# Kernel optimization log

Hardware: AMD Instinct MI355X
Metric: run time of the kernel (lower is better)

Reference implementation:

```python
import jax, jax.numpy as jnp
import numpy as np

N, E, B = 50000, 600000, 64
C_IN, H, C_OUT, L = 128, 128, 64, 3
BN_EPS = 1e-5


def setup_inputs() -> dict:
    key = jax.random.key(0)
    ks = iter(jax.random.split(key, 40))

    def w(shape, fan_in):
        return jax.random.normal(next(ks), shape, jnp.float32) / np.sqrt(fan_in).astype(np.float32)

    return {
        "x": jax.random.normal(next(ks), (N, C_IN), jnp.float32),
        "edge_index": jax.random.randint(next(ks), (2, E), 0, N),
        "batch": jnp.sort(jax.random.randint(next(ks), (N,), 0, B)),
        # GINConv MLPs: Linear(in,h) -> BN -> ReLU -> Linear(h,h)   (stacked over L; C_IN == H)
        "convW1": w((L, C_IN, H), C_IN), "convb1": jnp.zeros((L, H), jnp.float32),
        "bn_g": jnp.ones((L, H), jnp.float32), "bn_b": jnp.zeros((L, H), jnp.float32),
        "convW2": w((L, H, H), H), "convb2": jnp.zeros((L, H), jnp.float32),
        # reconstruction head: Linear(h,h)-ReLU-Linear(h,h)-ReLU-Linear(h,4)-ReLU
        "recW1": w((H, H), H), "recb1": jnp.zeros((H,), jnp.float32),
        "recW2": w((H, H), H), "recb2": jnp.zeros((H,), jnp.float32),
        "recW3": w((H, 4), H), "recb3": jnp.zeros((4,), jnp.float32),
        # final MLP([h,h,out], norm=None): Linear(h,h)-ReLU-(dropout, eval=identity)-Linear(h,out)
        "mlpW1": w((H, H), H), "mlpb1": jnp.zeros((H,), jnp.float32),
        "mlpW2": w((H, C_OUT), H), "mlpb2": jnp.zeros((C_OUT,), jnp.float32),
    }


def reference(x, edge_index, batch, convW1, convb1, bn_g, bn_b, convW2, convb2,
              recW1, recb1, recW2, recb2, recW3, recb3, mlpW1, mlpb1, mlpW2, mlpb2):
    src, dst = edge_index[0], edge_index[1]
    for l in range(L):
        # GIN aggregation: out_i = nn((1+eps)*x_i + sum_{j->i} x_j), eps = 0
        agg = jax.ops.segment_sum(x[src], dst, num_segments=N)  # [N, d]
        h = (x + agg) @ convW1[l] + convb1[l]                   # [N, H]
        mu = h.mean(axis=0)
        var = jnp.var(h, axis=0)                                # biased, torch BN train mode
        h = bn_g[l] * (h - mu) * jax.lax.rsqrt(var + BN_EPS) + bn_b[l]
        h = jax.nn.relu(h) @ convW2[l] + convb2[l]
        x = jax.nn.relu(h)                                      # outer .relu() in forward
    # reconstruction branch on node features
    x_rec = jax.nn.relu(x @ recW1 + recb1)
    x_rec = jax.nn.relu(x_rec @ recW2 + recb2)
    x_rec = jax.nn.relu(x_rec @ recW3 + recb3)                  # [N, 4]
    # global_add_pool keyed by graph id
    pooled = jax.ops.segment_sum(x, batch, num_segments=B)      # [B, H]
    out = jax.nn.relu(pooled @ mlpW1 + mlpb1) @ mlpW2 + mlpb2   # [B, C_OUT]
    return (out, x_rec)
```

## Files before the change

kernel.cpp:

```cpp
#include <hip/hip_runtime.h>

#define NN 50000
#define EE 600000
#define BB 64
#define CH 128
#define LL 3
#define NGB 391
#define NSB 196
#define NPB 392

typedef unsigned short u16;
typedef unsigned int u32;
typedef short s16x8 __attribute__((ext_vector_type(8)));
typedef float f32x4 __attribute__((ext_vector_type(4)));

__device__ __forceinline__ u16 f2b(float f) {
    u32 x = __float_as_uint(f);
    return (u16)((x + 0x7FFFu + ((x >> 16) & 1u)) >> 16);
}
__device__ __forceinline__ float b2f(u16 u) {
    return __uint_as_float(((u32)u) << 16);
}

__global__ __launch_bounds__(256) void k_zero2(int* __restrict__ deg,
                                               float* __restrict__ pooled,
                                               float* __restrict__ gstats,
                                               int* __restrict__ bar) {
    int i = blockIdx.x * 256 + threadIdx.x;
    if (i < NN) deg[i] = 0;
    int j = i - NN;
    if (j >= 0 && j < BB * CH) pooled[j] = 0.f;
    int k = j - BB * CH;
    if (k >= 0 && k < 3 * 256) gstats[k] = 0.f;
    int l = k - 3 * 256;
    if (l >= 0 && l < 4) bar[l] = 0;
}

__global__ __launch_bounds__(256) void k_count(const int* __restrict__ ei,
                                               int* __restrict__ deg) {
    int e = blockIdx.x * 256 + threadIdx.x;
    if (e < EE) atomicAdd(&deg[ei[EE + e]], 1);
}

__global__ __launch_bounds__(256) void k_scanA(const int* __restrict__ deg,
                                               int* __restrict__ bsum) {
    __shared__ int sm[256];
    int i = blockIdx.x * 256 + threadIdx.x;
    sm[threadIdx.x] = (i < NN) ? deg[i] : 0;
    __syncthreads();
    for (int off = 128; off > 0; off >>= 1) {
        if (threadIdx.x < off) sm[threadIdx.x] += sm[threadIdx.x + off];
        __syncthreads();
    }
    if (threadIdx.x == 0) bsum[blockIdx.x] = sm[0];
}

__global__ __launch_bounds__(256) void k_scanB(const int* __restrict__ deg,
                                               const int* __restrict__ bsum,
                                               int* __restrict__ rowptr,
                                               int* __restrict__ cur) {
    __shared__ int sb[256], sd[256];
    int t = threadIdx.x;
    sb[t] = (t < NSB) ? bsum[t] : 0;
    __syncthreads();
    for (int off = 1; off < 256; off <<= 1) {
        int v = (t >= off) ? sb[t - off] : 0;
        __syncthreads();
        sb[t] += v;
        __syncthreads();
    }
    int blockOff = (blockIdx.x == 0) ? 0 : sb[blockIdx.x - 1];
    int i = blockIdx.x * 256 + t;
    int d = (i < NN) ? deg[i] : 0;
    sd[t] = d;
    __syncthreads();
    for (int off = 1; off < 256; off <<= 1) {
        int v = (t >= off) ? sd[t - off] : 0;
        __syncthreads();
        sd[t] += v;
        __syncthreads();
    }
    int excl = blockOff + sd[t] - d;
    if (i < NN) { rowptr[i] = excl; cur[i] = excl; }
    if (i == NN - 1) rowptr[NN] = excl + d;
}

__global__ __launch_bounds__(256) void k_fill(const int* __restrict__ ei,
                                              int* __restrict__ cur,
                                              int* __restrict__ perm) {
    int e = blockIdx.x * 256 + threadIdx.x;
    if (e < EE) {
        int dst = ei[EE + e];
        int idx = atomicAdd(&cur[dst], 1);
        perm[idx] = ei[e];
    }
}

__global__ __launch_bounds__(256) void k_cvt(const float* __restrict__ x,
                                             u16* __restrict__ y) {
    long base = (long)(blockIdx.x * 256 + threadIdx.x) * 8;
    if (base < (long)NN * CH) {
        float4 f0 = *(const float4*)(x + base);
        float4 f1 = *(const float4*)(x + base + 4);
        union { u16 pk[8]; uint4 v; } uu;
        uu.pk[0] = f2b(f0.x); uu.pk[1] = f2b(f0.y);
        uu.pk[2] = f2b(f0.z); uu.pk[3] = f2b(f0.w);
        uu.pk[4] = f2b(f1.x); uu.pk[5] = f2b(f1.y);
        uu.pk[6] = f2b(f1.z); uu.pk[7] = f2b(f1.w);
        *(uint4*)(y + base) = uu.v;
    }
}

__global__ __launch_bounds__(256) void k_gather(const u16* __restrict__ x,
                                                const int* __restrict__ rowptr,
                                                const int* __restrict__ perm,
                                                u16* __restrict__ y) {
    int dst = blockIdx.x * 16 + (threadIdx.x >> 4);
    if (dst >= NN) return;
    int lane = threadIdx.x & 15;
    int co = lane * 8;
    int beg = rowptr[dst], end = rowptr[dst + 1];
    union { u16 pk[8]; uint4 v; } uu;
    uu.v = *(const uint4*)(x + (long)dst * CH + co);
    float a[8], b[8];
#pragma unroll
    for (int j = 0; j < 8; ++j) { a[j] = b2f(uu.pk[j]); b[j] = 0.f; }
    int e = beg;
    for (; e + 1 < end; e += 2) {
        int s0 = perm[e], s1 = perm[e + 1];
        union { u16 pk[8]; uint4 v; } v0, v1;
        v0.v = *(const uint4*)(x + (long)s0 * CH + co);
        v1.v = *(const uint4*)(x + (long)s1 * CH + co);
#pragma unroll
        for (int j = 0; j < 8; ++j) { a[j] += b2f(v0.pk[j]); b[j] += b2f(v1.pk[j]); }
    }
    if (e < end) {
        int s0 = perm[e];
        union { u16 pk[8]; uint4 v; } v0;
        v0.v = *(const uint4*)(x + (long)s0 * CH + co);
#pragma unroll
        for (int j = 0; j < 8; ++j) a[j] += b2f(v0.pk[j]);
    }
    union { u16 pk[8]; uint4 v; } ov;
#pragma unroll
    for (int j = 0; j < 8; ++j) ov.pk[j] = f2b(a[j] + b[j]);
    *(uint4*)(y + (long)dst * CH + co) = ov.v;
}

__global__ __launch_bounds__(256) void k_transpose_all(
    const float* __restrict__ cW1, const float* __restrict__ cW2,
    const float* __restrict__ rW1, const float* __restrict__ rW2,
    const float* __restrict__ rW3, u16* __restrict__ Wt) {
    int idx = blockIdx.x * 256 + threadIdx.x;
    if (idx < 8 * 16384) {
        int slot = idx >> 14;
        int wi = idx & 16383;
        int k = wi >> 7, n = wi & 127;
        const float* src = slot < 3 ? cW1 + slot * 16384
                         : slot < 6 ? cW2 + (slot - 3) * 16384
                         : slot == 6 ? rW1 : rW2;
        Wt[slot * 16384 + n * 128 + k] = f2b(src[wi]);
    } else if (idx < 9 * 16384) {
        int j = idx - 8 * 16384;
        int n = j >> 7, k = j & 127;
        Wt[8 * 16384 + j] = (n < 4) ? f2b(rW3[k * 4 + n]) : (u16)0;
    }
}

__device__ __forceinline__ void stageB8(const u16* __restrict__ Wt, u16* sB,
                                        int s, int rr) {
#pragma unroll
    for (int it = 0; it < 8; ++it) {
        int n = it * 16 + rr;
        uint4 u = *(const uint4*)(Wt + n * CH + 8 * s);
        *(uint4*)(&sB[n * CH + ((s ^ (n & 15)) * 8)]) = u;
    }
}

__device__ __forceinline__ void mfma8(const u16* sA, const u16* sB,
                                      f32x4 acc[2][8], int wv, int quad, int l16) {
    f32x4 z = {0.f, 0.f, 0.f, 0.f};
#pragma unroll
    for (int m = 0; m < 2; ++m)
#pragma unroll
        for (int t = 0; t < 8; ++t) acc[m][t] = z;
    const u16* pa0 = sA + (wv * 32 + l16) * CH;
    const u16* pa1 = pa0 + 16 * CH;
#pragma unroll
    for (int kc = 0; kc < 4; ++kc) {
        int off = (((kc << 2) | quad) ^ l16) << 3;
        s16x8 a0 = *(const s16x8*)(pa0 + off);
        s16x8 a1 = *(const s16x8*)(pa1 + off);
#pragma unroll
        for (int t = 0; t < 8; ++t) {
            s16x8 bfr = *(const s16x8*)(sB + (t * 16 + l16) * CH + off);
            acc[0][t] = __builtin_amdgcn_mfma_f32_16x16x32_bf16(a0, bfr, acc[0][t], 0, 0, 0);
            acc[1][t] = __builtin_amdgcn_mfma_f32_16x16x32_bf16(a1, bfr, acc[1][t], 0, 0, 0);
        }
    }
}

__device__ __forceinline__ void biasrelu(f32x4 acc[2][8],
                                         const float* __restrict__ bias, int l16) {
#pragma unroll
    for (int t = 0; t < 8; ++t) {
        float bv = bias[t * 16 + l16];
#pragma unroll
        for (int m = 0; m < 2; ++m)
#pragma unroll
            for (int r = 0; r < 4; ++r)
                acc[m][t][r] = fmaxf(acc[m][t][r] + bv, 0.f);
    }
}

__device__ __forceinline__ void restage(const f32x4 acc[2][8], u16* sA,
                                        int wv, int quad, int l16) {
#pragma unroll
    for (int t = 0; t < 8; ++t) {
        int chunk = (t << 1) | (l16 >> 3);
        int o7 = l16 & 7;
#pragma unroll
        for (int m = 0; m < 2; ++m)
#pragma unroll
            for (int r = 0; r < 4; ++r) {
                int lr = wv * 32 + m * 16 + quad * 4 + r;
                sA[lr * CH + ((chunk ^ (lr & 15)) << 3) + o7] = f2b(acc[m][t][r]);
            }
    }
}

__device__ __forceinline__ void grid_barrier(int* bar, int tid) {
    __syncthreads();
    if (tid == 0) {
        __hip_atomic_fetch_add(bar, 1, __ATOMIC_ACQ_REL, __HIP_MEMORY_SCOPE_AGENT);
        while (__hip_atomic_load(bar, __ATOMIC_ACQUIRE, __HIP_MEMORY_SCOPE_AGENT) < NGB) {
            __builtin_amdgcn_s_sleep(8);
        }
    }
    __syncthreads();
}

template <bool LAST>
__global__ __launch_bounds__(256, 2) void k_layer(
    const u16* __restrict__ y16, const u16* __restrict__ Wt, int layer,
    const float* __restrict__ cb1, const float* __restrict__ cb2,
    const float* __restrict__ g, const float* __restrict__ bbeta,
    float* __restrict__ gstats, int* __restrict__ bar, u16* __restrict__ xc,
    const float* __restrict__ rb1, const float* __restrict__ rb2,
    const float* __restrict__ rb3, float* __restrict__ x_rec) {
    __shared__ u16 sA[128 * CH];
    __shared__ u16 sB[128 * CH];
    const int tid = threadIdx.x;
    const int s = tid & 15, rr = tid >> 4;
    const int r0 = blockIdx.x * 128;
    const int lane = tid & 63, wv = tid >> 6, quad = lane >> 4, l16 = lane & 15;

    stageB8(Wt + layer * 16384, sB, s, rr);
#pragma unroll
    for (int it = 0; it < 8; ++it) {
        int lr = it * 16 + rr, gr = r0 + lr;
        union { u16 pk[8]; uint4 v; } uu;
        if (gr < NN) {
            uu.v = *(const uint4*)(y16 + (long)gr * CH + 8 * s);
        } else {
#pragma unroll
            for (int j = 0; j < 8; ++j) uu.pk[j] = 0;
        }
        *(uint4*)(&sA[lr * CH + ((s ^ (lr & 15)) * 8)]) = uu.v;
    }
    __syncthreads();
    f32x4 acc[2][8];
    mfma8(sA, sB, acc, wv, quad, l16);

    float ss[8], qq[8];
#pragma unroll
    for (int t = 0; t < 8; ++t) {
        float bv = cb1[t * 16 + l16];
        ss[t] = 0.f; qq[t] = 0.f;
#pragma unroll
        for (int m = 0; m < 2; ++m) {
            int rbase = r0 + wv * 32 + m * 16 + quad * 4;
#pragma unroll
            for (int r = 0; r < 4; ++r) {
                float v = acc[m][t][r] + bv;
                acc[m][t][r] = v;
                if (rbase + r < NN) { ss[t] += v; qq[t] += v * v; }
            }
        }
    }
#pragma unroll
    for (int t = 0; t < 8; ++t) {
        ss[t] += __shfl_xor(ss[t], 16);
        ss[t] += __shfl_xor(ss[t], 32);
        qq[t] += __shfl_xor(qq[t], 16);
        qq[t] += __shfl_xor(qq[t], 32);
    }
    float* red = (float*)sA;
    __syncthreads();
    if (lane < 16) {
#pragma unroll
        for (int t = 0; t < 8; ++t) {
            red[wv * 256 + t * 16 + l16] = ss[t];
            red[wv * 256 + 128 + t * 16 + l16] = qq[t];
        }
    }
    __syncthreads();
    unsafeAtomicAdd(&gstats[tid],
                    red[tid] + red[256 + tid] + red[512 + tid] + red[768 + tid]);

    grid_barrier(bar, tid);

#pragma unroll
    for (int t = 0; t < 8; ++t) {
        int col = t * 16 + l16;
        float sum = __hip_atomic_load(&gstats[col], __ATOMIC_RELAXED,
                                      __HIP_MEMORY_SCOPE_AGENT);
        float sq = __hip_atomic_load(&gstats[128 + col], __ATOMIC_RELAXED,
                                     __HIP_MEMORY_SCOPE_AGENT);
        float mu = sum / (float)NN;
        float var = sq / (float)NN - mu * mu;
        float rstd = rsqrtf(var + 1e-5f);
        float sc = g[col] * rstd;
        float sh = bbeta[col] - mu * sc;
#pragma unroll
        for (int m = 0; m < 2; ++m)
#pragma unroll
            for (int r = 0; r < 4; ++r)
                acc[m][t][r] = fmaxf(acc[m][t][r] * sc + sh, 0.f);
    }

    __syncthreads();
    restage(acc, sA, wv, quad, l16);
    stageB8(Wt + (3 + layer) * 16384, sB, s, rr);
    __syncthreads();
    mfma8(sA, sB, acc, wv, quad, l16);
    biasrelu(acc, cb2, l16);
#pragma unroll
    for (int t = 0; t < 8; ++t) {
        int col = t * 16 + l16;
#pragma unroll
        for (int m = 0; m < 2; ++m)
#pragma unroll
            for (int r = 0; r < 4; ++r) {
                int row = r0 + wv * 32 + m * 16 + quad * 4 + r;
                if (row < NN) xc[(long)row * CH + col] = f2b(acc[m][t][r]);
            }
    }

    if constexpr (LAST) {
        __syncthreads();
        restage(acc, sA, wv, quad, l16);
        stageB8(Wt + 6 * 16384, sB, s, rr);
        __syncthreads();
        mfma8(sA, sB, acc, wv, quad, l16);
        biasrelu(acc, rb1, l16);
        __syncthreads();
        restage(acc, sA, wv, quad, l16);
        stageB8(Wt + 7 * 16384, sB, s, rr);
        __syncthreads();
        mfma8(sA, sB, acc, wv, quad, l16);
        biasrelu(acc, rb2, l16);
        __syncthreads();
        restage(acc, sA, wv, quad, l16);
        {
            int n = rr;
            uint4 u = *(const uint4*)(Wt + 8 * 16384 + n * CH + 8 * s);
            *(uint4*)(&sB[n * CH + ((s ^ (n & 15)) * 8)]) = u;
        }
        __syncthreads();
        f32x4 a4[2];
        a4[0] = (f32x4){0.f, 0.f, 0.f, 0.f};
        a4[1] = (f32x4){0.f, 0.f, 0.f, 0.f};
        const u16* pa0 = sA + (wv * 32 + l16) * CH;
        const u16* pa1 = pa0 + 16 * CH;
#pragma unroll
        for (int kc = 0; kc < 4; ++kc) {
            int off = (((kc << 2) | quad) ^ l16) << 3;
            s16x8 a0 = *(const s16x8*)(pa0 + off);
            s16x8 a1 = *(const s16x8*)(pa1 + off);
            s16x8 bfr = *(const s16x8*)(sB + l16 * CH + off);
            a4[0] = __builtin_amdgcn_mfma_f32_16x16x32_bf16(a0, bfr, a4[0], 0, 0, 0);
            a4[1] = __builtin_amdgcn_mfma_f32_16x16x32_bf16(a1, bfr, a4[1], 0, 0, 0);
        }
        if (l16 < 4) {
            float bv = rb3[l16];
#pragma unroll
            for (int m = 0; m < 2; ++m)
#pragma unroll
                for (int r = 0; r < 4; ++r) {
                    int row = r0 + wv * 32 + m * 16 + quad * 4 + r;
                    if (row < NN) x_rec[(long)row * 4 + l16] = fmaxf(a4[m][r] + bv, 0.f);
                }
        }
    }
}

__global__ __launch_bounds__(256) void k_pool(const u16* __restrict__ x,
                                              const int* __restrict__ batch,
                                              float* __restrict__ pooled) {
    int r0 = blockIdx.x * 128;
    if (r0 >= NN) return;
    int rend = r0 + 128 < NN ? r0 + 128 : NN;
    int c = threadIdx.x & 127;
    int half = threadIdx.x >> 7;
    int r = r0 + half;
    if (r >= rend) return;
    int g = batch[r];
    float s = 0.f;
    for (; r < rend; r += 2) {
        int gg = batch[r];
        if (gg != g) {
            unsafeAtomicAdd(pooled + g * CH + c, s);
            s = 0.f;
            g = gg;
        }
        s += b2f(x[(long)r * CH + c]);
    }
    unsafeAtomicAdd(pooled + g * CH + c, s);
}

__global__ __launch_bounds__(128) void k_mlp(const float* __restrict__ pooled,
                                             const float* __restrict__ W1,
                                             const float* __restrict__ b1,
                                             const float* __restrict__ W2,
                                             const float* __restrict__ b2,
                                             float* __restrict__ out) {
    __shared__ float p[128], t1[128];
    int b = blockIdx.x, t = threadIdx.x;
    p[t] = pooled[b * CH + t];
    __syncthreads();
    float acc = b1[t];
    for (int k = 0; k < 128; ++k) acc += p[k] * W1[k * 128 + t];
    t1[t] = fmaxf(acc, 0.f);
    __syncthreads();
    if (t < 64) {
        float o = b2[t];
        for (int k = 0; k < 128; ++k) o += t1[k] * W2[k * 64 + t];
        out[b * 64 + t] = o;
    }
}

extern "C" void kernel_launch(void* const* d_in, const int* in_sizes, int n_in,
                              void* d_out, int out_size, void* d_ws, size_t ws_size,
                              hipStream_t stream) {
    const float* x_in   = (const float*)d_in[0];
    const int*   ei     = (const int*)d_in[1];
    const int*   batch  = (const int*)d_in[2];
    const float* convW1 = (const float*)d_in[3];
    const float* convb1 = (const float*)d_in[4];
    const float* bn_g   = (const float*)d_in[5];
    const float* bn_b   = (const float*)d_in[6];
    const float* convW2 = (const float*)d_in[7];
    const float* convb2 = (const float*)d_in[8];
    const float* recW1  = (const float*)d_in[9];
    const float* recb1  = (const float*)d_in[10];
    const float* recW2  = (const float*)d_in[11];
    const float* recb2  = (const float*)d_in[12];
    const float* recW3  = (const float*)d_in[13];
    const float* recb3  = (const float*)d_in[14];
    const float* mlpW1  = (const float*)d_in[15];
    const float* mlpb1  = (const float*)d_in[16];
    const float* mlpW2  = (const float*)d_in[17];
    const float* mlpb2  = (const float*)d_in[18];

    float* out   = (float*)d_out;
    float* x_rec = out + 4096;

    char* w = (char*)d_ws;
    u16*   x16    = (u16*)w;    w += (size_t)NN * CH * 2;
    u16*   y16    = (u16*)w;    w += (size_t)NN * CH * 2;
    u16*   xc     = (u16*)w;    w += (size_t)NN * CH * 2;
    u16*   Wt     = (u16*)w;    w += (size_t)9 * 16384 * 2;
    float* gstats = (float*)w;  w += (size_t)3 * 256 * 4;
    int*   bar    = (int*)w;    w += 4 * 4;
    float* pooled = (float*)w;  w += (size_t)BB * CH * 4;
    int*   deg    = (int*)w;    w += (size_t)NN * 4;
    int*   bsum   = (int*)w;    w += (size_t)NSB * 4;
    int*   rowptr = (int*)w;    w += (size_t)(NN + 1) * 4;
    int*   cur    = (int*)w;    w += (size_t)NN * 4;
    int*   perm   = (int*)w;    w += (size_t)EE * 4;

    dim3 b256(256), b128(128);

    k_zero2<<<231, b256, 0, stream>>>(deg, pooled, gstats, bar);
    k_count<<<2344, b256, 0, stream>>>(ei, deg);
    k_scanA<<<NSB, b256, 0, stream>>>(deg, bsum);
    k_scanB<<<NSB, b256, 0, stream>>>(deg, bsum, rowptr, cur);
    k_fill<<<2344, b256, 0, stream>>>(ei, cur, perm);
    k_cvt<<<3125, b256, 0, stream>>>(x_in, x16);
    k_transpose_all<<<576, b256, 0, stream>>>(convW1, convW2, recW1, recW2, recW3, Wt);

    const u16* cur_x = x16;
    for (int l = 0; l < LL; ++l) {
        k_gather<<<3125, b256, 0, stream>>>(cur_x, rowptr, perm, y16);
        if (l < LL - 1)
            k_layer<false><<<NGB, b256, 0, stream>>>(
                y16, Wt, l, convb1 + l * 128, convb2 + l * 128,
                bn_g + l * 128, bn_b + l * 128, gstats + l * 256, bar + l, xc,
                recb1, recb2, recb3, x_rec);
        else
            k_layer<true><<<NGB, b256, 0, stream>>>(
                y16, Wt, l, convb1 + l * 128, convb2 + l * 128,
                bn_g + l * 128, bn_b + l * 128, gstats + l * 256, bar + l, xc,
                recb1, recb2, recb3, x_rec);
        cur_x = xc;
    }
    k_pool<<<NPB, b256, 0, stream>>>(xc, batch, pooled);
    k_mlp<<<64, b128, 0, stream>>>(pooled, mlpW1, mlpb1, mlpW2, mlpb2, out);
}
```

Measured before the change: 428.5 us.

## Split fused layer kernel at BN barrier into two GEMM kernels

Replaces the persistent layer kernel's software grid barrier with a kernel boundary. The first kernel computes the first GEMM plus the BN statistics and writes pre-BN activations to global memory as bf16. The second kernel applies the BN scale/shift and ReLU while loading those activations, then runs the second GEMM. This removes the spin-wait grid barrier and its co-residency requirement, at the cost of an extra launch and a full round trip of the activations through global memory.

```diff
diff --git a/kernel.cpp b/kernel.cpp
--- a/kernel.cpp
+++ b/kernel.cpp
@@ -24,16 +24,13 @@
 
 __global__ __launch_bounds__(256) void k_zero2(int* __restrict__ deg,
                                                float* __restrict__ pooled,
-                                               float* __restrict__ gstats,
-                                               int* __restrict__ bar) {
+                                               float* __restrict__ gstats) {
     int i = blockIdx.x * 256 + threadIdx.x;
     if (i < NN) deg[i] = 0;
     int j = i - NN;
     if (j >= 0 && j < BB * CH) pooled[j] = 0.f;
     int k = j - BB * CH;
     if (k >= 0 && k < 3 * 256) gstats[k] = 0.f;
-    int l = k - 3 * 256;
-    if (l >= 0 && l < 4) bar[l] = 0;
 }
 
 __global__ __launch_bounds__(256) void k_count(const int* __restrict__ ei,
@@ -229,25 +226,9 @@
     }
 }
 
-__device__ __forceinline__ void grid_barrier(int* bar, int tid) {
-    __syncthreads();
-    if (tid == 0) {
-        __hip_atomic_fetch_add(bar, 1, __ATOMIC_ACQ_REL, __HIP_MEMORY_SCOPE_AGENT);
-        while (__hip_atomic_load(bar, __ATOMIC_ACQUIRE, __HIP_MEMORY_SCOPE_AGENT) < NGB) {
-            __builtin_amdgcn_s_sleep(8);
-        }
-    }
-    __syncthreads();
-}
-
-template <bool LAST>
-__global__ __launch_bounds__(256, 2) void k_layer(
-    const u16* __restrict__ y16, const u16* __restrict__ Wt, int layer,
-    const float* __restrict__ cb1, const float* __restrict__ cb2,
-    const float* __restrict__ g, const float* __restrict__ bbeta,
-    float* __restrict__ gstats, int* __restrict__ bar, u16* __restrict__ xc,
-    const float* __restrict__ rb1, const float* __restrict__ rb2,
-    const float* __restrict__ rb3, float* __restrict__ x_rec) {
+__global__ __launch_bounds__(256, 2) void k_gemm1(
+    u16* __restrict__ hy, const u16* __restrict__ Wt, int layer,
+    const float* __restrict__ cb1, float* __restrict__ gstats) {
     __shared__ u16 sA[128 * CH];
     __shared__ u16 sB[128 * CH];
     const int tid = threadIdx.x;
@@ -261,7 +242,7 @@
         int lr = it * 16 + rr, gr = r0 + lr;
         union { u16 pk[8]; uint4 v; } uu;
         if (gr < NN) {
-            uu.v = *(const uint4*)(y16 + (long)gr * CH + 8 * s);
+            uu.v = *(const uint4*)(hy + (long)gr * CH + 8 * s);
         } else {
 #pragma unroll
             for (int j = 0; j < 8; ++j) uu.pk[j] = 0;
@@ -308,31 +289,67 @@
     unsafeAtomicAdd(&gstats[tid],
                     red[tid] + red[256 + tid] + red[512 + tid] + red[768 + tid]);
 
-    grid_barrier(bar, tid);
-
 #pragma unroll
     for (int t = 0; t < 8; ++t) {
         int col = t * 16 + l16;
-        float sum = __hip_atomic_load(&gstats[col], __ATOMIC_RELAXED,
-                                      __HIP_MEMORY_SCOPE_AGENT);
-        float sq = __hip_atomic_load(&gstats[128 + col], __ATOMIC_RELAXED,
-                                     __HIP_MEMORY_SCOPE_AGENT);
+#pragma unroll
+        for (int m = 0; m < 2; ++m)
+#pragma unroll
+            for (int r = 0; r < 4; ++r) {
+                int row = r0 + wv * 32 + m * 16 + quad * 4 + r;
+                if (row < NN) hy[(long)row * CH + col] = f2b(acc[m][t][r]);
+            }
+    }
+}
+
+template <bool LAST>
+__global__ __launch_bounds__(256, 2) void k_gemm2(
+    const u16* __restrict__ h16, const u16* __restrict__ Wt, int layer,
+    const float* __restrict__ g, const float* __restrict__ bbeta,
+    const float* __restrict__ gstats, const float* __restrict__ cb2,
+    u16* __restrict__ xc,
+    const float* __restrict__ rb1, const float* __restrict__ rb2,
+    const float* __restrict__ rb3, float* __restrict__ x_rec) {
+    __shared__ u16 sA[128 * CH];
+    __shared__ u16 sB[128 * CH];
+    __shared__ float snorm[256];
+    const int tid = threadIdx.x;
+    const int s = tid & 15, rr = tid >> 4;
+    const int r0 = blockIdx.x * 128;
+    const int lane = tid & 63, wv = tid >> 6, quad = lane >> 4, l16 = lane & 15;
+
+    if (tid < 128) {
+        float sum = gstats[tid];
+        float sq = gstats[128 + tid];
         float mu = sum / (float)NN;
         float var = sq / (float)NN - mu * mu;
-        float rstd = rsqrtf(var + 1e-5f);
-        float sc = g[col] * rstd;
-        float sh = bbeta[col] - mu * sc;
-#pragma unroll
-        for (int m = 0; m < 2; ++m)
-#pragma unroll
-            for (int r = 0; r < 4; ++r)
-                acc[m][t][r] = fmaxf(acc[m][t][r] * sc + sh, 0.f);
-    }
-
-    __syncthreads();
-    restage(acc, sA, wv, quad, l16);
+        float sc = g[tid] * rsqrtf(var + 1e-5f);
+        snorm[tid] = sc;
+        snorm[128 + tid] = bbeta[tid] - mu * sc;
+    }
     stageB8(Wt + (3 + layer) * 16384, sB, s, rr);
     __syncthreads();
+
+#pragma unroll
+    for (int it = 0; it < 8; ++it) {
+        int lr = it * 16 + rr, gr = r0 + lr;
+        union { u16 pk[8]; uint4 v; } uu;
+        if (gr < NN) {
+            uu.v = *(const uint4*)(h16 + (long)gr * CH + 8 * s);
+#pragma unroll
+            for (int j = 0; j < 8; ++j) {
+                int c = 8 * s + j;
+                float v = fmaxf(b2f(uu.pk[j]) * snorm[c] + snorm[128 + c], 0.f);
+                uu.pk[j] = f2b(v);
+            }
+        } else {
+#pragma unroll
+            for (int j = 0; j < 8; ++j) uu.pk[j] = 0;
+        }
+        *(uint4*)(&sA[lr * CH + ((s ^ (lr & 15)) * 8)]) = uu.v;
+    }
+    __syncthreads();
+    f32x4 acc[2][8];
     mfma8(sA, sB, acc, wv, quad, l16);
     biasrelu(acc, cb2, l16);
 #pragma unroll
@@ -472,7 +489,6 @@
     u16*   xc     = (u16*)w;    w += (size_t)NN * CH * 2;
     u16*   Wt     = (u16*)w;    w += (size_t)9 * 16384 * 2;
     float* gstats = (float*)w;  w += (size_t)3 * 256 * 4;
-    int*   bar    = (int*)w;    w += 4 * 4;
     float* pooled = (float*)w;  w += (size_t)BB * CH * 4;
     int*   deg    = (int*)w;    w += (size_t)NN * 4;
     int*   bsum   = (int*)w;    w += (size_t)NSB * 4;
@@ -482,7 +498,7 @@
 
     dim3 b256(256), b128(128);
 
-    k_zero2<<<231, b256, 0, stream>>>(deg, pooled, gstats, bar);
+    k_zero2<<<231, b256, 0, stream>>>(deg, pooled, gstats);
     k_count<<<2344, b256, 0, stream>>>(ei, deg);
     k_scanA<<<NSB, b256, 0, stream>>>(deg, bsum);
     k_scanB<<<NSB, b256, 0, stream>>>(deg, bsum, rowptr, cur);
@@ -493,16 +509,16 @@
     const u16* cur_x = x16;
     for (int l = 0; l < LL; ++l) {
         k_gather<<<3125, b256, 0, stream>>>(cur_x, rowptr, perm, y16);
+        k_gemm1<<<NGB, b256, 0, stream>>>(y16, Wt, l, convb1 + l * 128,
+                                          gstats + l * 256);
         if (l < LL - 1)
-            k_layer<false><<<NGB, b256, 0, stream>>>(
-                y16, Wt, l, convb1 + l * 128, convb2 + l * 128,
-                bn_g + l * 128, bn_b + l * 128, gstats + l * 256, bar + l, xc,
-                recb1, recb2, recb3, x_rec);
+            k_gemm2<false><<<NGB, b256, 0, stream>>>(
+                y16, Wt, l, bn_g + l * 128, bn_b + l * 128, gstats + l * 256,
+                convb2 + l * 128, xc, recb1, recb2, recb3, x_rec);
         else
-            k_layer<true><<<NGB, b256, 0, stream>>>(
-                y16, Wt, l, convb1 + l * 128, convb2 + l * 128,
-                bn_g + l * 128, bn_b + l * 128, gstats + l * 256, bar + l, xc,
-                recb1, recb2, recb3, x_rec);
+            k_gemm2<true><<<NGB, b256, 0, stream>>>(
+                y16, Wt, l, bn_g + l * 128, bn_b + l * 128, gstats + l * 256,
+                convb2 + l * 128, xc, recb1, recb2, recb3, x_rec);
         cur_x = xc;
     }
     k_pool<<<NPB, b256, 0, stream>>>(xc, batch, pooled);
```

Measured after the change: 383.0 us. 10.6% less time.
